# Performance work log

Hardware: AMD Instinct MI355X
Metric: run time of the kernel (lower is better)

Reference implementation:

```python
import jax, jax.numpy as jnp
import numpy as np

BASE_RES = 192          # image_shape = [192, 192]
VIEWS = 128             # radial views
READOUT_OS = 2.0        # readout oversampling
SAMPLES = int(BASE_RES * READOUT_OS)  # 384 samples per spoke


def _radial_traj_and_weights():
    """Linear-ordered full-range 2D radial trajectory + ramp density weights."""
    t = jnp.arange(SAMPLES, dtype=jnp.float32)
    # radius spans [-pi, pi) along each spoke (NUFFT convention)
    r = (t - SAMPLES / 2) / (SAMPLES / 2) * jnp.pi            # [samples]
    theta = jnp.arange(VIEWS, dtype=jnp.float32) * (jnp.pi / VIEWS)  # [views]
    kx = r[None, :] * jnp.cos(theta)[:, None]                 # [views, samples]
    ky = r[None, :] * jnp.sin(theta)[:, None]
    points = jnp.stack([kx, ky], axis=-1).reshape(-1, 2)      # [M, 2]
    # geometric (ramp) density compensation: weight ~ |k| with DC floor
    rho = jnp.abs(r) / jnp.pi                                 # [samples], in [0, 1]
    w = jnp.maximum(rho, 1.0 / SAMPLES)                       # avoid zero at DC
    weights = jnp.broadcast_to(w[None, :], (VIEWS, SAMPLES)).reshape(-1)  # [M]
    return points, weights


def setup_inputs() -> dict:
    key = jax.random.key(0)
    x = jax.random.normal(key, (2, BASE_RES, BASE_RES, 2), dtype=jnp.float32)
    points, weights = _radial_traj_and_weights()
    return {"x": x, "points": points, "weights": weights}


def _nudft_resample(xc, points, weights):
    """Type-2 NUDFT (forward) -> density comp -> type-1 NUDFT (adjoint).

    xc: complex [C, B, H, W]; points: [M, 2] in [-pi, pi); weights: [M].
    The 2D nonuniform DFT phase factorizes per axis: exp(-i(kx*nx + ky*ny)).
    """
    C, B, H, W = xc.shape
    nx = (jnp.arange(H, dtype=jnp.float32) - H // 2)          # grid indices
    ny = (jnp.arange(W, dtype=jnp.float32) - W // 2)
    Ax = jnp.exp(-1j * (points[:, 0:1] * nx[None, :]).astype(jnp.complex64))  # [M, H]
    Ay = jnp.exp(-1j * (points[:, 1:2] * ny[None, :]).astype(jnp.complex64))  # [M, W]
    # type-2: k[m] = sum_{h,w} x[h,w] exp(-i(kx_m h + ky_m w))
    tmp = jnp.einsum('cbhw,mh->cbmw', xc, Ax)                 # [C, B, M, W]
    k = jnp.einsum('cbmw,mw->cbm', tmp, Ay)                   # [C, B, M]
    # density compensation
    k = k * weights.astype(jnp.complex64)
    # type-1 adjoint: img[h,w] = sum_m k[m] exp(+i(kx_m h + ky_m w))
    tmp2 = jnp.einsum('cbm,mh->cbmh', k, jnp.conj(Ax))        # [C, B, M, H]
    img = jnp.einsum('cbmh,mw->cbhw', tmp2, jnp.conj(Ay))     # [C, B, H, W]
    # scale by 1 / num_elements(image_shape)
    return img / jnp.asarray(H * W, dtype=jnp.complex64)


def reference(x, points, weights):
    # inputs [B, H, W, C] -> channels-first [C, B, H, W] (layer's perm)
    rank = x.ndim
    perm = [rank - 1] + list(range(rank - 1))
    xc = jnp.transpose(x, perm).astype(jnp.complex64)
    img = _nudft_resample(xc, points, weights)
    out = jnp.abs(img)                                        # layer dtype is real
    inv_perm = list(range(1, rank)) + [0]
    return jnp.transpose(out, inv_perm)                       # [B, H, W, C]
```

## Files before the change

### kernel.cpp

```cpp
#include <hip/hip_runtime.h>
#include <math.h>


#define HH 192
#define WW 192
#define NVIEWS 128
#define NSAMP 384
#define NPIX (HH*WW)
#define HALFT 193
#define M2 12545
#define M2P 12672
#define KTOT 25344
#define NSPLITK 33

typedef __attribute__((ext_vector_type(8))) short bf16x8;
typedef __attribute__((ext_vector_type(4))) float f32x4;
typedef __attribute__((ext_vector_type(8))) unsigned short u16x8;

__device__ __forceinline__ void rot(float& cr, float& ci, float dr, float di) {
  float nr = cr*dr - ci*di;
  float ni = cr*di + ci*dr;
  cr = nr; ci = ni;
}
__device__ __forceinline__ unsigned short f2b(float f) {
  unsigned int u = __float_as_uint(f);
  u += 0x7fffu + ((u >> 16) & 1u);
  return (unsigned short)(u >> 16);
}
__device__ __forceinline__ float b2f(unsigned short h) {
  return __uint_as_float(((unsigned int)h) << 16);
}

__global__ __launch_bounds__(256) void phase_kernel(
    const float* __restrict__ points, unsigned short* __restrict__ BT,
    unsigned short* __restrict__ CxT, unsigned short* __restrict__ SxT,
    unsigned short* __restrict__ Am) {
  const int v2 = blockIdx.x;
  const int role = blockIdx.y;
  const int t = threadIdx.x;
  if (t >= HALFT) return;
  if (role < 4) {
    const int hsplit = role;
    const float kx = points[(v2*NSAMP + t)*2 + 0];
    const int m2 = v2*HALFT + t;
    const int h0 = hsplit*48;
    float cr, ci; __sincosf(kx*(float)(h0-96), &ci, &cr);
    float dr, di; __sincosf(kx, &di, &dr);
    u16x8 pc, ps;
    for (int j = 0; j < 48; ++j) {
      const int h = h0 + j;
      CxT[(size_t)h*M2P + m2] = f2b(cr);
      SxT[(size_t)h*M2P + m2] = f2b(ci);
      pc[j&7] = f2b(cr); ps[j&7] = f2b(ci);
      if ((j&7) == 7) {
        *(u16x8*)(Am + (size_t)m2*192 + (h-7))         = pc;
        *(u16x8*)(Am + (size_t)(12672+m2)*192 + (h-7)) = ps;
      }
      rot(cr, ci, dr, di);
    }
  } else {
    const int wsplit = role - 4;
    const float ky = points[(v2*NSAMP + t)*2 + 1];
    const int kap = v2*HALFT + t;
    const int w0 = wsplit*48;
    float cr, ci; __sincosf(ky*(float)(w0-96), &ci, &cr);
    float dr, di; __sincosf(ky, &di, &dr);
    for (int j = 0; j < 48; ++j) {
      BT[(size_t)(w0+j)*KTOT + kap]       = f2b(cr);
      BT[(size_t)(w0+j)*KTOT + M2P + kap] = f2b(ci);
      rot(cr, ci, dr, di);
    }
  }
}


__global__ __launch_bounds__(256) void xprep_kernel(
    const float* __restrict__ x, unsigned short* __restrict__ XT) {
  const int idx = blockIdx.x*256 + threadIdx.x;
  if (idx >= 768*192) return;
  const int n = idx / 192, h = idx - n*192;
  const int cb = n / 192, w = n - cb*192;
  const int b = cb >> 1, c = cb & 1;
  XT[idx] = f2b(x[(((size_t)b*HH + h)*WW + w)*2 + c]);
}

__global__ __launch_bounds__(256) void gemm1_kernel(
    const unsigned short* __restrict__ Am, const unsigned short* __restrict__ XT,
    const float* __restrict__ points, float* __restrict__ Abuf) {
  __shared__ float lds[2][128][2];
  const int mt = blockIdx.x;
  const int cb = blockIdx.y;
  const int wv = threadIdx.x >> 6;
  const int lane = threadIdx.x & 63;
  const int r = lane & 15, kg = lane >> 4;
  const int mhalf = wv >> 1;
  const int whalf = wv & 1;
  const int mbase = mt*128 + mhalf*64;
  const int wbase = whalf*96;
  const int nbase = cb*192 + wbase;

  f32x4 acc[4][6];
  #pragma unroll
  for (int a = 0; a < 4; ++a)
    #pragma unroll
    for (int b = 0; b < 6; ++b) acc[a][b] = (f32x4){0.f,0.f,0.f,0.f};

  const unsigned short* Ap = Am + (size_t)(mbase + r)*192 + kg*8;
  const unsigned short* Bp = XT + (size_t)(nbase + r)*192 + kg*8;
  #pragma unroll
  for (int ks = 0; ks < 6; ++ks) {
    bf16x8 af[4], bfr[6];
    #pragma unroll
    for (int mf = 0; mf < 4; ++mf)
      af[mf] = *(const bf16x8*)(Ap + (size_t)mf*16*192 + ks*32);
    #pragma unroll
    for (int nf = 0; nf < 6; ++nf)
      bfr[nf] = *(const bf16x8*)(Bp + (size_t)nf*16*192 + ks*32);
    #pragma unroll
    for (int mf = 0; mf < 4; ++mf)
      #pragma unroll
      for (int nf = 0; nf < 6; ++nf)
        acc[mf][nf] = __builtin_amdgcn_mfma_f32_16x16x32_bf16(
            af[mf], bfr[nf], acc[mf][nf], 0, 0, 0);
  }

  const bool isCx = (mt < 99);
  const int m2w = mbase - (isCx ? 0 : 12672);
  float accA[16], accB[16];
  #pragma unroll
  for (int mf = 0; mf < 4; ++mf)
    #pragma unroll
    for (int reg = 0; reg < 4; ++reg) {
      const int m2 = m2w + mf*16 + kg*4 + reg;
      const int v2 = m2 / HALFT, t = m2 - v2*HALFT;
      const float ky = points[(v2*NSAMP + t)*2 + 1];
      float a0 = 0.f, b0 = 0.f;
      #pragma unroll
      for (int nf = 0; nf < 6; ++nf) {
        const float wo = (float)(wbase + nf*16 + r - 96);
        float sy, cy; __sincosf(ky*wo, &sy, &cy);
        const float g = acc[mf][nf][reg];
        a0 = fmaf(g, cy, a0);
        b0 = fmaf(g, sy, b0);
      }
      accA[mf*4+reg] = a0; accB[mf*4+reg] = b0;
    }
  #pragma unroll
  for (int msk = 1; msk <= 8; msk <<= 1) {
    #pragma unroll
    for (int i = 0; i < 16; ++i) {
      accA[i] += __shfl_xor(accA[i], msk);
      accB[i] += __shfl_xor(accB[i], msk);
    }
  }
  if (r == 0) {
    #pragma unroll
    for (int mf = 0; mf < 4; ++mf)
      #pragma unroll
      for (int reg = 0; reg < 4; ++reg) {
        const int mloc = mhalf*64 + mf*16 + kg*4 + reg;
        lds[whalf][mloc][0] = accA[mf*4+reg];
        lds[whalf][mloc][1] = accB[mf*4+reg];
      }
  }
  __syncthreads();
  {
    const int tid = threadIdx.x;
    const int mloc = tid >> 1, slot = tid & 1;
    const float val = lds[0][mloc][slot] + lds[1][mloc][slot];
    const int m2 = mt*128 + mloc - (isCx ? 0 : 12672);
    const int idx = isCx ? (slot ? 3 : 0) : (slot ? 1 : 2);
    Abuf[((size_t)cb*M2P + m2)*4 + idx] = val;
  }
}

__global__ __launch_bounds__(256) void combine2_kernel(
    const float* __restrict__ Abuf, const float* __restrict__ weights,
    float* __restrict__ combos, float* __restrict__ K2edge) {
  const int m2 = blockIdx.x*256 + threadIdx.x;
  if (m2 >= M2) return;
  const int v2 = m2 / HALFT, t = m2 - v2*HALFT;
  float f = weights[t] * (1.0f/36864.0f);
  if (t != 0 && t != 192) f *= 2.0f;
  const bool hp = (v2 >= 1 && v2 <= 63);
  #pragma unroll
  for (int cb = 0; cb < 4; ++cb) {
    const float4 A = *(const float4*)(Abuf + ((size_t)cb*M2P + m2)*4);
    const float A1 = A.x, A2 = A.y, A3 = A.z, A4 = A.w;
    float c0, c1, c2, c3;
    if (hp) {
      c0 =  2.f*f*A1; c1 = -2.f*f*A2; c2 = -2.f*f*A4; c3 = -2.f*f*A3;
    } else {
      const float kr = f*(A1 - A2), ki = -f*(A3 + A4);
      c0 = kr; c1 = kr; c2 = ki; c3 = ki;
    }
    combos[(cb*4+0)*M2P + m2] = c0;
    combos[(cb*4+1)*M2P + m2] = c1;
    combos[(cb*4+2)*M2P + m2] = c2;
    combos[(cb*4+3)*M2P + m2] = c3;
    if (t == 0 || t == 192) {
      const int d = (t == 0) ? 0 : 1;
      float* e = K2edge + ((v2*2 + d)*4 + cb)*2;
      e[0] = f*(A1 - A2); e[1] = -f*(A3 + A4);
      if (hp) {
        float* e2 = K2edge + (((128 - v2)*2 + d)*4 + cb)*2;
        e2[0] = f*(A1 + A2); e2[1] = f*(A3 - A4);
      }
    }
  }
}


__global__ __launch_bounds__(256) void tmat_kernel(
    const float* __restrict__ combos, const unsigned short* __restrict__ CxT,
    const unsigned short* __restrict__ SxT, unsigned short* __restrict__ A) {
  const int m2 = blockIdx.x*256 + threadIdx.x;
  if (m2 >= M2P) return;
  const int j = blockIdx.y;
  unsigned short* Arow = A + (size_t)j*KTOT;
  if (m2 >= M2) { Arow[m2] = 0; Arow[M2P + m2] = 0; return; }
  const int cb = j / 192, h = j - cb*192;
  const float cx = b2f(CxT[(size_t)h*M2P + m2]);
  const float sx = b2f(SxT[(size_t)h*M2P + m2]);
  const float c0 = combos[(cb*4+0)*M2P + m2];
  const float c1 = combos[(cb*4+1)*M2P + m2];
  const float c2 = combos[(cb*4+2)*M2P + m2];
  const float c3 = combos[(cb*4+3)*M2P + m2];
  Arow[m2]       = f2b(c0*cx - c3*sx);
  Arow[M2P + m2] = f2b(-(c1*sx + c2*cx));
}

__global__ __launch_bounds__(256) void adj_gemm(
    const unsigned short* __restrict__ A, const unsigned short* __restrict__ BT,
    float* __restrict__ partials) {
  const int mt = blockIdx.x;
  const int kc = blockIdx.y;
  const int wv = threadIdx.x >> 6;
  const int lane = threadIdx.x & 63;
  const int r = lane & 15, kg = lane >> 4;
  const int jbase = mt*128 + (wv>>1)*64;
  const int wbase = (wv&1)*96;
  const int kb = kc*768 + kg*8;

  f32x4 acc[4][6];
  #pragma unroll
  for (int a = 0; a < 4; ++a)
    #pragma unroll
    for (int b = 0; b < 6; ++b) acc[a][b] = (f32x4){0.f,0.f,0.f,0.f};

  const unsigned short* Ap = A + (size_t)(jbase + r)*KTOT + kb;
  const unsigned short* Bp = BT + (size_t)(wbase + r)*KTOT + kb;
  for (int ks = 0; ks < 24; ++ks) {
    bf16x8 af[4], bfr[6];
    #pragma unroll
    for (int mf = 0; mf < 4; ++mf)
      af[mf] = *(const bf16x8*)(Ap + (size_t)mf*16*KTOT + ks*32);
    #pragma unroll
    for (int nf = 0; nf < 6; ++nf)
      bfr[nf] = *(const bf16x8*)(Bp + (size_t)nf*16*KTOT + ks*32);
    #pragma unroll
    for (int mf = 0; mf < 4; ++mf)
      #pragma unroll
      for (int nf = 0; nf < 6; ++nf)
        acc[mf][nf] = __builtin_amdgcn_mfma_f32_16x16x32_bf16(
            af[mf], bfr[nf], acc[mf][nf], 0, 0, 0);
  }
  float* base = partials + (size_t)kc*192*768;
  #pragma unroll
  for (int mf = 0; mf < 4; ++mf)
    #pragma unroll
    for (int nf = 0; nf < 6; ++nf) {
      const int w = wbase + nf*16 + r;
      const int j = jbase + mf*16 + kg*4;
      *(f32x4*)(base + (size_t)w*768 + j) = acc[mf][nf];
    }
}

__global__ __launch_bounds__(256) void im_kernel(
    const unsigned short* __restrict__ BT, const unsigned short* __restrict__ CxT,
    const unsigned short* __restrict__ SxT, const float* __restrict__ K2edge,
    float* __restrict__ imb) {
  __shared__ float cxs[65][8], sxs[65][8], cys[65][8], sys[65][8];
  __shared__ float red[4][64][4];
  const int bx = blockIdx.x;
  const int h0 = (bx/24)*8, w0 = (bx%24)*8;
  const int tid = threadIdx.x;
  for (int i = tid; i < 65*8; i += 256) {
    const int v2 = i >> 3, e = i & 7;
    const int kap = v2*HALFT;
    cxs[v2][e] = b2f(CxT[(size_t)(h0+e)*M2P + kap]);
    sxs[v2][e] = b2f(SxT[(size_t)(h0+e)*M2P + kap]);
    cys[v2][e] = b2f(BT[(size_t)(w0+e)*KTOT + kap]);
    sys[v2][e] = b2f(BT[(size_t)(w0+e)*KTOT + M2P + kap]);
  }
  __syncthreads();
  const int g = tid >> 6, hi = (tid >> 3) & 7, wi = tid & 7;
  float im[4] = {0,0,0,0};
  for (int v = g*32; v < g*32 + 32; ++v) {
    const int v2 = (v <= 64) ? v : 128 - v;
    const float sg = (v <= 64) ? 1.f : -1.f;
    const float cx = cxs[v2][hi], sx = sg*sxs[v2][hi];
    const float cy = cys[v2][wi], sy = sys[v2][wi];
    const float t1 = cx*sy + sx*cy;
    const float t2 = cx*cy - sx*sy;
    const int idx = v*16;
    #pragma unroll
    for (int cb = 0; cb < 4; ++cb)
      im[cb] += K2edge[idx + cb*2]*t1 + K2edge[idx + cb*2 + 1]*t2;
  }
  const int p = tid & 63;
  #pragma unroll
  for (int cb = 0; cb < 4; ++cb) red[g][p][cb] = im[cb];
  __syncthreads();
  if (g == 0) {
    #pragma unroll
    for (int cb = 0; cb < 4; ++cb)
      im[cb] += red[1][p][cb] + red[2][p][cb] + red[3][p][cb];
    const int pix = (h0+hi)*192 + (w0+wi);
    *(float4*)(imb + pix*4) = make_float4(im[0], im[1], im[2], im[3]);
  }
}

__global__ __launch_bounds__(256) void out_new_kernel(
    const float* __restrict__ partials, const float* __restrict__ imb,
    float* __restrict__ out) {
  const int g = blockIdx.x*256 + threadIdx.x;
  const int w = g / 768, cbh = g - w*768;
  const int cb = cbh / 192, h = cbh - cb*192;
  float re = 0.f;
  for (int kc = 0; kc < NSPLITK; ++kc)
    re += partials[(size_t)kc*147456 + g];
  const float im = imb[(h*192 + w)*4 + cb];
  const float mag = sqrtf(re*re + im*im);
  const int b = cb >> 1, c = cb & 1;
  out[((size_t)b*NPIX + h*192 + w)*2 + c] = mag;
}


template <int HPER>
__global__ __launch_bounds__(192) void fwd_kernel(
    const float* __restrict__ x, const float* __restrict__ points,
    float* __restrict__ kpart) {
  const int v = blockIdx.x;
  const int split = blockIdx.y;
  const int t = threadIdx.x;
  const int m = v*NSAMP + t;
  const float kx = points[2*m+0];
  const float ky = points[2*m+1];
  const int h0 = split*HPER;

  float kr[4] = {0,0,0,0}, ki[4] = {0,0,0,0};
  float cyr, cyi; __sincosf(96.0f*ky, &cyi, &cyr);
  float dyr, dyi; __sincosf(-ky, &dyi, &dyr);
  float cx0r, cx0i; __sincosf(kx*(float)(96-h0), &cx0i, &cx0r);
  float dxr, dxi; __sincosf(-kx, &dxi, &dxr);

  for (int wp = 0; wp < 96; ++wp) {
    const int w0 = wp*2;
    float g0r[4]={0,0,0,0}, g0i[4]={0,0,0,0};
    float g1r[4]={0,0,0,0}, g1i[4]={0,0,0,0};
    float cxr = cx0r, cxi = cx0i;
    const float* p0 = x + (h0*WW + w0)*2;
    const float* p1 = p0 + HH*WW*2;
    #pragma unroll 4
    for (int h = 0; h < HPER; ++h) {
      float4 a = *(const float4*)(p0 + h*(WW*2));
      float4 b = *(const float4*)(p1 + h*(WW*2));
      g0r[0] += a.x*cxr; g0i[0] += a.x*cxi;
      g0r[1] += a.y*cxr; g0i[1] += a.y*cxi;
      g1r[0] += a.z*cxr; g1i[0] += a.z*cxi;
      g1r[1] += a.w*cxr; g1i[1] += a.w*cxi;
      g0r[2] += b.x*cxr; g0i[2] += b.x*cxi;
      g0r[3] += b.y*cxr; g0i[3] += b.y*cxi;
      g1r[2] += b.z*cxr; g1i[2] += b.z*cxi;
      g1r[3] += b.w*cxr; g1i[3] += b.w*cxi;
      rot(cxr, cxi, dxr, dxi);
    }
    #pragma unroll
    for (int cb = 0; cb < 4; ++cb) {
      kr[cb] += g0r[cb]*cyr - g0i[cb]*cyi;
      ki[cb] += g0r[cb]*cyi + g0i[cb]*cyr;
    }
    rot(cyr, cyi, dyr, dyi);
    #pragma unroll
    for (int cb = 0; cb < 4; ++cb) {
      kr[cb] += g1r[cb]*cyr - g1i[cb]*cyi;
      ki[cb] += g1r[cb]*cyi + g1i[cb]*cyr;
    }
    rot(cyr, cyi, dyr, dyi);
  }
  float* o = kpart + (((split*NVIEWS + v)*192 + t)*4)*2;
  #pragma unroll
  for (int cb = 0; cb < 4; ++cb) { o[2*cb] = kr[cb]; o[2*cb+1] = ki[cb]; }
}

__global__ __launch_bounds__(256) void dc_kernel(
    const float* __restrict__ x, float* __restrict__ dcsum) {
  const int tid = threadIdx.x;
  float s0=0.f, s1=0.f, s2=0.f, s3=0.f;
  for (int i = tid; i < NPIX; i += 256) {
    float2 a = *(const float2*)(x + i*2);
    float2 b = *(const float2*)(x + HH*WW*2 + i*2);
    s0 += a.x; s1 += a.y; s2 += b.x; s3 += b.y;
  }
  #pragma unroll
  for (int off = 32; off > 0; off >>= 1) {
    s0 += __shfl_down(s0, off);
    s1 += __shfl_down(s1, off);
    s2 += __shfl_down(s2, off);
    s3 += __shfl_down(s3, off);
  }
  __shared__ float red[4][4];
  const int wv = tid >> 6, ln = tid & 63;
  if (ln == 0) { red[0][wv]=s0; red[1][wv]=s1; red[2][wv]=s2; red[3][wv]=s3; }
  __syncthreads();
  if (tid < 4) {
    float tot = red[tid][0]+red[tid][1]+red[tid][2]+red[tid][3];
    dcsum[2*tid] = tot; dcsum[2*tid+1] = 0.0f;
  }
}

__global__ __launch_bounds__(256) void combine_kernel(
    const float* __restrict__ kpart, const float* __restrict__ dcsum,
    const float* __restrict__ weights, float* __restrict__ K2, int nsplit) {
  const int idx = blockIdx.x*256 + threadIdx.x;
  if (idx >= NVIEWS*HALFT) return;
  const int v = idx / HALFT, t = idx % HALFT;
  float f = weights[t] * (1.0f/36864.0f);
  if (t != 0 && t != 192) f *= 2.0f;
  float o[8];
  if (t == 192) {
    #pragma unroll
    for (int cb = 0; cb < 4; ++cb) { o[2*cb] = f*dcsum[2*cb]; o[2*cb+1] = f*dcsum[2*cb+1]; }
  } else {
    #pragma unroll
    for (int cb = 0; cb < 4; ++cb) {
      float ar = 0.f, ai = 0.f;
      for (int s = 0; s < nsplit; ++s) {
        const float* p = kpart + (((s*NVIEWS + v)*192 + t)*4 + cb)*2;
        ar += p[0]; ai += p[1];
      }
      o[2*cb] = f*ar; o[2*cb+1] = f*ai;
    }
  }
  float* q = K2 + idx*8;
  #pragma unroll
  for (int j = 0; j < 8; ++j) q[j] = o[j];
}

template <int VPC>
__global__ __launch_bounds__(256) void adj_kernel(
    const float* __restrict__ K2, const float* __restrict__ points,
    float* __restrict__ imgpart) {
  const int pix = blockIdx.x*256 + threadIdx.x;
  const int chunk = blockIdx.y;
  const float nh = (float)(pix / WW - 96);
  const float nw = (float)(pix % WW - 96);
  float re[4] = {0,0,0,0}, im[4] = {0,0,0,0};
  const float INVPI = 0.3183098861837907f;
  const float PI192 = 3.14159265358979f / 192.0f;
  for (int v = chunk*VPC; v < chunk*VPC + VPC; ++v) {
    const float ct = -points[2*(v*NSAMP)+0] * INVPI;
    const float st = -points[2*(v*NSAMP)+1] * INVPI;
    const float alpha = ct*nh + st*nw;
    const float delta = alpha * PI192;
    float dr, di; __sincosf(delta, &di, &dr);
    float c0r, c0i; __sincosf(-192.0f*delta, &c0i, &c0r);
    const float* Kv = K2 + v*HALFT*8;
    #pragma unroll
    for (int cb = 0; cb < 4; ++cb) {
      float a = Kv[2*cb], b = Kv[2*cb+1];
      re[cb] += a*c0r - b*c0i;
      im[cb] += a*c0i + b*c0r;
    }
    float d2r = dr*dr - di*di, d2i = 2.0f*dr*di;
    float ar = c0r*dr - c0i*di, ai = c0r*di + c0i*dr;
    float br = ar*dr - ai*di,  bi = ar*di + ai*dr;
    for (int i = 0; i < 95; ++i) {
      const float* ka = Kv + (2*i+1)*8;
      const float* kb = Kv + (2*i+2)*8;
      #pragma unroll
      for (int cb = 0; cb < 4; ++cb)
        re[cb] += ka[2*cb]*ar - ka[2*cb+1]*ai;
      #pragma unroll
      for (int cb = 0; cb < 4; ++cb)
        re[cb] += kb[2*cb]*br - kb[2*cb+1]*bi;
      rot(ar, ai, d2r, d2i);
      rot(br, bi, d2r, d2i);
    }
    {
      const float* ka = Kv + 191*8;
      #pragma unroll
      for (int cb = 0; cb < 4; ++cb)
        re[cb] += ka[2*cb]*ar - ka[2*cb+1]*ai;
    }
    const float* kd = Kv + 192*8;
    #pragma unroll
    for (int cb = 0; cb < 4; ++cb) { re[cb] += kd[2*cb]; im[cb] += kd[2*cb+1]; }
  }
  float* o = imgpart + (chunk*NPIX + pix)*8;
  #pragma unroll
  for (int cb = 0; cb < 4; ++cb) { o[2*cb] = re[cb]; o[2*cb+1] = im[cb]; }
}

__global__ __launch_bounds__(256) void out_fb_kernel(
    const float* __restrict__ imgpart, float* __restrict__ out, int nchunk) {
  const int pix = blockIdx.x*256 + threadIdx.x;
  float re[4] = {0,0,0,0}, im[4] = {0,0,0,0};
  for (int ch = 0; ch < nchunk; ++ch) {
    const float* p = imgpart + (ch*NPIX + pix)*8;
    #pragma unroll
    for (int cb = 0; cb < 4; ++cb) { re[cb] += p[2*cb]; im[cb] += p[2*cb+1]; }
  }
  #pragma unroll
  for (int b = 0; b < 2; ++b)
    #pragma unroll
    for (int c = 0; c < 2; ++c) {
      const int cb = b*2 + c;
      out[(b*NPIX + pix)*2 + c] = sqrtf(re[cb]*re[cb] + im[cb]*im[cb]);
    }
}

extern "C" void kernel_launch(void* const* d_in, const int* in_sizes, int n_in,
                              void* d_out, int out_size, void* d_ws, size_t ws_size,
                              hipStream_t stream) {
  const float* x       = (const float*)d_in[0];
  const float* points  = (const float*)d_in[1];
  const float* weights = (const float*)d_in[2];
  float* out = (float*)d_out;

  const size_t NEED = 79265792ull;
  if (ws_size >= NEED) {
    char* wsb = (char*)d_ws;
    unsigned short* BT   = (unsigned short*)(wsb + 0);
    unsigned short* CxT  = (unsigned short*)(wsb + 9732096);
    unsigned short* SxT  = (unsigned short*)(wsb + 14598144);
    float* combos        = (float*)(wsb + 19464192);
    float* K2edge        = (float*)(wsb + 20275200);
    char* S              = wsb + 20283392;
    unsigned short* Am   = (unsigned short*)(S + 0);
    unsigned short* XT   = (unsigned short*)(S + 9732096);
    float* Abuf          = (float*)(S + 10027008);
    unsigned short* Aadj = (unsigned short*)(S + 0);
    float* partials      = (float*)(S + 38928384);
    float* imb           = (float*)(S + 58392576);

    phase_kernel<<<dim3(65,8), 256, 0, stream>>>(points, BT, CxT, SxT, Am);
    xprep_kernel<<<576, 256, 0, stream>>>(x, XT);
    gemm1_kernel<<<dim3(198,4), 256, 0, stream>>>(Am, XT, points, Abuf);
    combine2_kernel<<<(M2 + 255)/256, 256, 0, stream>>>(
        Abuf, weights, combos, K2edge);
    tmat_kernel<<<dim3((M2P + 255)/256, 768), 256, 0, stream>>>(
        combos, CxT, SxT, Aadj);
    adj_gemm<<<dim3(6, NSPLITK), 256, 0, stream>>>(Aadj, BT, partials);
    im_kernel<<<576, 256, 0, stream>>>(BT, CxT, SxT, K2edge, imb);
    out_new_kernel<<<(192*768)/256, 256, 0, stream>>>(partials, imb, out);
  } else {
    float* ws = (float*)d_ws;
    const size_t ws_floats = ws_size / sizeof(float);
    int nsplit = 16, nchunk = 16;
    auto need = [&](int ns, int nc) -> size_t {
      return (size_t)ns*196608 + 8 + 197632 + (size_t)nc*294912;
    };
    while (need(nsplit, nchunk) > ws_floats && nchunk > 1) nchunk >>= 1;
    while (need(nsplit, nchunk) > ws_floats && nsplit > 1) nsplit >>= 1;

    float* kpart   = ws;
    float* dcsum   = kpart + (size_t)nsplit*196608;
    float* K2      = dcsum + 8;
    float* imgpart = K2 + 197632;

    switch (nsplit) {
      case 16: fwd_kernel<12><<<dim3(NVIEWS,16), 192, 0, stream>>>(x, points, kpart); break;
      case 8:  fwd_kernel<24><<<dim3(NVIEWS,8),  192, 0, stream>>>(x, points, kpart); break;
      case 4:  fwd_kernel<48><<<dim3(NVIEWS,4),  192, 0, stream>>>(x, points, kpart); break;
      case 2:  fwd_kernel<96><<<dim3(NVIEWS,2),  192, 0, stream>>>(x, points, kpart); break;
      default: fwd_kernel<192><<<dim3(NVIEWS,1), 192, 0, stream>>>(x, points, kpart); break;
    }
    dc_kernel<<<1, 256, 0, stream>>>(x, dcsum);
    combine_kernel<<<(NVIEWS*HALFT + 255)/256, 256, 0, stream>>>(
        kpart, dcsum, weights, K2, nsplit);
    switch (nchunk) {
      case 16: adj_kernel<8>  <<<dim3(NPIX/256,16), 256, 0, stream>>>(K2, points, imgpart); break;
      case 8:  adj_kernel<16> <<<dim3(NPIX/256,8),  256, 0, stream>>>(K2, points, imgpart); break;
      case 4:  adj_kernel<32> <<<dim3(NPIX/256,4),  256, 0, stream>>>(K2, points, imgpart); break;
      case 2:  adj_kernel<64> <<<dim3(NPIX/256,2),  256, 0, stream>>>(K2, points, imgpart); break;
      default: adj_kernel<128><<<dim3(NPIX/256,1),  256, 0, stream>>>(K2, points, imgpart); break;
    }
    out_fb_kernel<<<NPIX/256, 256, 0, stream>>>(imgpart, out, nchunk);
  }
}
```

Measured before the change: 137.3 us.

## Fuse adjoint A-matrix generation into adj_gemm, dropping tmat kernel

Removes the tmat_kernel that materialized a 768x25344 bf16 adjoint matrix in global memory. adj_gemm now builds A fragments on the fly from combos and the CxT/SxT phase tables, and combine2 writes combos in a sign-rearranged form (zero-padding the tail) so a single FMA pair suffices. The adj_gemm tile is also reshaped to 2 waves/64 rows with twice as many blocks. This saves the large write and reread of A but adds per-k-step scattered loads and conversion ALU work inside the GEMM loop.

```diff
diff --git a/kernel.cpp b/kernel.cpp
--- a/kernel.cpp
+++ b/kernel.cpp
@@ -178,7 +178,12 @@
     const float* __restrict__ Abuf, const float* __restrict__ weights,
     float* __restrict__ combos, float* __restrict__ K2edge) {
   const int m2 = blockIdx.x*256 + threadIdx.x;
-  if (m2 >= M2) return;
+  if (m2 >= M2P) return;
+  if (m2 >= M2) {
+    #pragma unroll
+    for (int q = 0; q < 16; ++q) combos[(size_t)q*M2P + m2] = 0.f;
+    return;
+  }
   const int v2 = m2 / HALFT, t = m2 - v2*HALFT;
   float f = weights[t] * (1.0f/36864.0f);
   if (t != 0 && t != 192) f *= 2.0f;
@@ -187,17 +192,17 @@
   for (int cb = 0; cb < 4; ++cb) {
     const float4 A = *(const float4*)(Abuf + ((size_t)cb*M2P + m2)*4);
     const float A1 = A.x, A2 = A.y, A3 = A.z, A4 = A.w;
-    float c0, c1, c2, c3;
+    float p0, p1, q0, q1;
     if (hp) {
-      c0 =  2.f*f*A1; c1 = -2.f*f*A2; c2 = -2.f*f*A4; c3 = -2.f*f*A3;
+      p0 = 2.f*f*A1; p1 = 2.f*f*A3; q0 = 2.f*f*A4; q1 = 2.f*f*A2;
     } else {
       const float kr = f*(A1 - A2), ki = -f*(A3 + A4);
-      c0 = kr; c1 = kr; c2 = ki; c3 = ki;
-    }
-    combos[(cb*4+0)*M2P + m2] = c0;
-    combos[(cb*4+1)*M2P + m2] = c1;
-    combos[(cb*4+2)*M2P + m2] = c2;
-    combos[(cb*4+3)*M2P + m2] = c3;
+      p0 = kr; p1 = -ki; q0 = -ki; q1 = -kr;
+    }
+    combos[(size_t)(cb*4+0)*M2P + m2] = p0;
+    combos[(size_t)(cb*4+1)*M2P + m2] = p1;
+    combos[(size_t)(cb*4+2)*M2P + m2] = q0;
+    combos[(size_t)(cb*4+3)*M2P + m2] = q1;
     if (t == 0 || t == 192) {
       const int d = (t == 0) ? 0 : 1;
       float* e = K2edge + ((v2*2 + d)*4 + cb)*2;
@@ -210,36 +215,17 @@
   }
 }
 
-
-__global__ __launch_bounds__(256) void tmat_kernel(
+__global__ __launch_bounds__(128) void adj_gemm(
     const float* __restrict__ combos, const unsigned short* __restrict__ CxT,
-    const unsigned short* __restrict__ SxT, unsigned short* __restrict__ A) {
-  const int m2 = blockIdx.x*256 + threadIdx.x;
-  if (m2 >= M2P) return;
-  const int j = blockIdx.y;
-  unsigned short* Arow = A + (size_t)j*KTOT;
-  if (m2 >= M2) { Arow[m2] = 0; Arow[M2P + m2] = 0; return; }
-  const int cb = j / 192, h = j - cb*192;
-  const float cx = b2f(CxT[(size_t)h*M2P + m2]);
-  const float sx = b2f(SxT[(size_t)h*M2P + m2]);
-  const float c0 = combos[(cb*4+0)*M2P + m2];
-  const float c1 = combos[(cb*4+1)*M2P + m2];
-  const float c2 = combos[(cb*4+2)*M2P + m2];
-  const float c3 = combos[(cb*4+3)*M2P + m2];
-  Arow[m2]       = f2b(c0*cx - c3*sx);
-  Arow[M2P + m2] = f2b(-(c1*sx + c2*cx));
-}
-
-__global__ __launch_bounds__(256) void adj_gemm(
-    const unsigned short* __restrict__ A, const unsigned short* __restrict__ BT,
+    const unsigned short* __restrict__ SxT, const unsigned short* __restrict__ BT,
     float* __restrict__ partials) {
   const int mt = blockIdx.x;
   const int kc = blockIdx.y;
   const int wv = threadIdx.x >> 6;
   const int lane = threadIdx.x & 63;
   const int r = lane & 15, kg = lane >> 4;
-  const int jbase = mt*128 + (wv>>1)*64;
-  const int wbase = (wv&1)*96;
+  const int jbase = mt*64;
+  const int wbase = wv*96;
   const int kb = kc*768 + kg*8;
 
   f32x4 acc[4][6];
@@ -248,22 +234,41 @@
     #pragma unroll
     for (int b = 0; b < 6; ++b) acc[a][b] = (f32x4){0.f,0.f,0.f,0.f};
 
-  const unsigned short* Ap = A + (size_t)(jbase + r)*KTOT + kb;
   const unsigned short* Bp = BT + (size_t)(wbase + r)*KTOT + kb;
   for (int ks = 0; ks < 24; ++ks) {
-    bf16x8 af[4], bfr[6];
-    #pragma unroll
-    for (int mf = 0; mf < 4; ++mf)
-      af[mf] = *(const bf16x8*)(Ap + (size_t)mf*16*KTOT + ks*32);
+    bf16x8 bfr[6];
     #pragma unroll
     for (int nf = 0; nf < 6; ++nf)
       bfr[nf] = *(const bf16x8*)(Bp + (size_t)nf*16*KTOT + ks*32);
-    #pragma unroll
-    for (int mf = 0; mf < 4; ++mf)
+
+    const int kap = kb + ks*32;
+    const bool isQ = (kap >= M2P);
+    const int m2b = kap - (isQ ? M2P : 0);
+    const int off = isQ ? 2 : 0;
+
+    #pragma unroll
+    for (int mf = 0; mf < 4; ++mf) {
+      const int j = jbase + mf*16 + r;
+      const int cb = j / 192;
+      const int h  = j - cb*192;
+      const u16x8 cxv = *(const u16x8*)(CxT + (size_t)h*M2P + m2b);
+      const u16x8 sxv = *(const u16x8*)(SxT + (size_t)h*M2P + m2b);
+      const float* crow = combos + (size_t)(cb*4 + off)*M2P + m2b;
+      float ccos[8], csin[8];
+      *(float4*)&ccos[0] = *(const float4*)(crow);
+      *(float4*)&ccos[4] = *(const float4*)(crow + 4);
+      *(float4*)&csin[0] = *(const float4*)(crow + M2P);
+      *(float4*)&csin[4] = *(const float4*)(crow + M2P + 4);
+      u16x8 av;
+      #pragma unroll
+      for (int e = 0; e < 8; ++e)
+        av[e] = f2b(ccos[e]*b2f(cxv[e]) + csin[e]*b2f(sxv[e]));
+      const bf16x8 af = *(const bf16x8*)&av;
       #pragma unroll
       for (int nf = 0; nf < 6; ++nf)
         acc[mf][nf] = __builtin_amdgcn_mfma_f32_16x16x32_bf16(
-            af[mf], bfr[nf], acc[mf][nf], 0, 0, 0);
+            af, bfr[nf], acc[mf][nf], 0, 0, 0);
+    }
   }
   float* base = partials + (size_t)kc*192*768;
   #pragma unroll
@@ -541,18 +546,16 @@
     unsigned short* Am   = (unsigned short*)(S + 0);
     unsigned short* XT   = (unsigned short*)(S + 9732096);
     float* Abuf          = (float*)(S + 10027008);
-    unsigned short* Aadj = (unsigned short*)(S + 0);
     float* partials      = (float*)(S + 38928384);
     float* imb           = (float*)(S + 58392576);
 
     phase_kernel<<<dim3(65,8), 256, 0, stream>>>(points, BT, CxT, SxT, Am);
     xprep_kernel<<<576, 256, 0, stream>>>(x, XT);
     gemm1_kernel<<<dim3(198,4), 256, 0, stream>>>(Am, XT, points, Abuf);
-    combine2_kernel<<<(M2 + 255)/256, 256, 0, stream>>>(
+    combine2_kernel<<<(M2P + 255)/256, 256, 0, stream>>>(
         Abuf, weights, combos, K2edge);
-    tmat_kernel<<<dim3((M2P + 255)/256, 768), 256, 0, stream>>>(
-        combos, CxT, SxT, Aadj);
-    adj_gemm<<<dim3(6, NSPLITK), 256, 0, stream>>>(Aadj, BT, partials);
+    adj_gemm<<<dim3(12, NSPLITK), 128, 0, stream>>>(
+        combos, CxT, SxT, BT, partials);
     im_kernel<<<576, 256, 0, stream>>>(BT, CxT, SxT, K2edge, imb);
     out_new_kernel<<<(192*768)/256, 256, 0, stream>>>(partials, imb, out);
   } else {
```

Result: slower. 150.8 us (+9.9%).
